# Optimization experiments

Measured on AMD Instinct MI355X. Metric: run time of the kernel, lower is better.

The kernel has to match this reference:

```python
import jax, jax.numpy as jnp
import numpy as np
from math import sqrt

B, S, F, H, FF, L = 16, 512, 512, 8, 2048, 3
HEAD_DIM = F // H
LN_EPS = 1e-5


def setup_inputs() -> dict:
    key = jax.random.key(0)
    ks = iter(jax.random.split(key, 80))

    def nrm(shape, scale=0.02):
        return jax.random.normal(next(ks), shape, jnp.float32) * scale

    inp = {
        "embedding": jax.random.normal(next(ks), (B, S, F), jnp.float32),
        "lengths": jax.random.randint(next(ks), (B,), 1, S + 1, dtype=jnp.int32),
    }
    for p in ("enc", "dec"):
        inp[p + "_wqkv"] = nrm((L, 3, F, F))
        inp[p + "_bqkv"] = nrm((L, 3, F))
        inp[p + "_wo"] = nrm((L, F, F))
        inp[p + "_bo"] = nrm((L, F))
        inp[p + "_ln1_g"] = jnp.ones((L, F), jnp.float32)
        inp[p + "_ln1_b"] = jnp.zeros((L, F), jnp.float32)
        inp[p + "_ff_w1"] = nrm((L, F, FF))
        inp[p + "_ff_b1"] = nrm((L, FF))
        inp[p + "_ff_w2"] = nrm((L, FF, F))
        inp[p + "_ff_b2"] = nrm((L, F))
        inp[p + "_ln2_g"] = jnp.ones((L, F), jnp.float32)
        inp[p + "_ln2_b"] = jnp.zeros((L, F), jnp.float32)
    inp["ptr_w_q"] = nrm((F,), 1.0)
    inp["ptr_w_k"] = nrm((F,), 1.0)
    return inp


def _ln(x, g, b):
    mu = x.mean(-1, keepdims=True)
    var = ((x - mu) ** 2).mean(-1, keepdims=True)
    return (x - mu) / jnp.sqrt(var + LN_EPS) * g + b


def _mha(q_in, kv_in, wqkv, bqkv, wo, bo, mask):
    # q_in [b,sq,f], kv_in [b,sk,f], mask broadcastable to [b,h,sq,sk] (True = masked)
    b, sq, f = q_in.shape
    q = q_in @ wqkv[0] + bqkv[0]
    k = kv_in @ wqkv[1] + bqkv[1]
    v = kv_in @ wqkv[2] + bqkv[2]

    def split(t):
        return t.reshape(t.shape[0], t.shape[1], H, HEAD_DIM).transpose(0, 2, 1, 3)

    q, k, v = split(q), split(k), split(v)  # [b,h,s,dh]
    scores = jnp.einsum("bhqd,bhkd->bhqk", q, k) / sqrt(HEAD_DIM)
    scores = jnp.where(mask, jnp.finfo(scores.dtype).min, scores)
    attn = jax.nn.softmax(scores, axis=-1)
    out = jnp.einsum("bhqk,bhkd->bhqd", attn, v)
    out = out.transpose(0, 2, 1, 3).reshape(b, sq, f)
    return out @ wo + bo


def _layer(x, mem, mask, wqkv, bqkv, wo, bo, ln1_g, ln1_b, w1, b1, w2, b2, ln2_g, ln2_b):
    x = _ln(x + _mha(x, mem, wqkv, bqkv, wo, bo, mask), ln1_g, ln1_b)
    ff = jax.nn.gelu(x @ w1 + b1, approximate=False) @ w2 + b2
    return _ln(x + ff, ln2_g, ln2_b)


def _forward(embedding, lengths,
             enc_wqkv, enc_bqkv, enc_wo, enc_bo, enc_ln1_g, enc_ln1_b,
             enc_ff_w1, enc_ff_b1, enc_ff_w2, enc_ff_b2, enc_ln2_g, enc_ln2_b,
             dec_wqkv, dec_bqkv, dec_wo, dec_bo, dec_ln1_g, dec_ln1_b,
             dec_ff_w1, dec_ff_b1, dec_ff_w2, dec_ff_b2, dec_ln2_g, dec_ln2_b,
             ptr_w_q, ptr_w_k):
    b, s, f = embedding.shape
    pos = jnp.arange(s)
    key_mask = pos[None, :] >= lengths[:, None]  # [b,s] True = padded

    # ---- encoder (self-attn with key padding mask) ----
    enc_mask = key_mask[:, None, None, :]  # [b,1,1,s]
    x = embedding
    for i in range(L):
        x = _layer(x, x, enc_mask,
                   enc_wqkv[i], enc_bqkv[i], enc_wo[i], enc_bo[i],
                   enc_ln1_g[i], enc_ln1_b[i],
                   enc_ff_w1[i], enc_ff_b1[i], enc_ff_w2[i], enc_ff_b2[i],
                   enc_ln2_g[i], enc_ln2_b[i])
    memory = x

    # ---- decoder: all timesteps batched (no recurrent state in original loop) ----
    # query t attends keys j < min(t, len); t=0 is overridden with zeros below
    # (key 0 left unmasked for t=0 only to keep softmax finite).
    t = jnp.arange(s)
    limit = jnp.minimum(jnp.maximum(t, 1)[None, :], lengths[:, None])  # [b,sq]
    dec_mask = (pos[None, None, :] >= limit[:, :, None])[:, None, :, :]  # [b,1,sq,sk]
    y = embedding
    for i in range(L):
        y = _layer(y, memory, dec_mask,
                   dec_wqkv[i], dec_bqkv[i], dec_wo[i], dec_bo[i],
                   dec_ln1_g[i], dec_ln1_b[i],
                   dec_ff_w1[i], dec_ff_b1[i], dec_ff_w2[i], dec_ff_b2[i],
                   dec_ln2_g[i], dec_ln2_b[i])

    # ---- pointer logits ----
    wq = y @ ptr_w_q        # [b, sq]
    wk = memory @ ptr_w_k   # [b, sk]
    ptr = jax.nn.sigmoid((wq[:, None, :] + wk[:, :, None]) / sqrt(f))  # [b, sk, sq]
    return jnp.where(t[None, None, :] == 0, 0.0, ptr)


def reference(embedding, lengths,
              enc_wqkv, enc_bqkv, enc_wo, enc_bo, enc_ln1_g, enc_ln1_b,
              enc_ff_w1, enc_ff_b1, enc_ff_w2, enc_ff_b2, enc_ln2_g, enc_ln2_b,
              dec_wqkv, dec_bqkv, dec_wo, dec_bo, dec_ln1_g, dec_ln1_b,
              dec_ff_w1, dec_ff_b1, dec_ff_w2, dec_ff_b2, dec_ln2_g, dec_ln2_b,
              ptr_w_q, ptr_w_k):
    return _forward(embedding, lengths,
                    enc_wqkv, enc_bqkv, enc_wo, enc_bo, enc_ln1_g, enc_ln1_b,
                    enc_ff_w1, enc_ff_b1, enc_ff_w2, enc_ff_b2, enc_ln2_g, enc_ln2_b,
                    dec_wqkv, dec_bqkv, dec_wo, dec_bo, dec_ln1_g, dec_ln1_b,
                    dec_ff_w1, dec_ff_b1, dec_ff_w2, dec_ff_b2, dec_ln2_g, dec_ln2_b,
                    ptr_w_q, ptr_w_k)
```

## Files before the change

### kernel.cpp

```cpp
#include <hip/hip_runtime.h>
#include <hip/hip_bf16.h>
#include <math.h>

#define TB 16
#define TS 512
#define TF 512
#define TH 8
#define TFF 2048
#define TL 3

typedef unsigned short u16;
typedef short bf16x8 __attribute__((ext_vector_type(8)));
typedef float f32x4 __attribute__((ext_vector_type(4)));

__device__ __forceinline__ u16 f2b(float f) {
    __hip_bfloat16 h = __float2bfloat16(f);
    return *reinterpret_cast<u16*>(&h);
}
__device__ __forceinline__ float b2f(u16 u) {
    unsigned int v = ((unsigned int)u) << 16;
    return __builtin_bit_cast(float, v);
}

__device__ __forceinline__ void gload_lds16(const void* g, void* l) {
    __builtin_amdgcn_global_load_lds(
        (const __attribute__((address_space(1))) unsigned int*)g,
        (__attribute__((address_space(3))) unsigned int*)l, 16, 0, 0);
}

__global__ __launch_bounds__(256) void k_transpose_w(
    const float* __restrict__ src, u16* __restrict__ dst, int K, int N)
{
    __shared__ float tile[32][33];
    const int z = blockIdx.z;
    src += (size_t)z * K * N;
    dst += (size_t)z * K * N;
    const int n0 = blockIdx.x * 32, k0 = blockIdx.y * 32;
    const int tx = threadIdx.x & 31, ty = threadIdx.x >> 5;
    #pragma unroll
    for (int i = 0; i < 32; i += 8)
        tile[ty + i][tx] = src[(size_t)(k0 + ty + i) * N + n0 + tx];
    __syncthreads();
    #pragma unroll
    for (int i = 0; i < 32; i += 8)
        dst[(size_t)(n0 + ty + i) * K + k0 + tx] = f2b(tile[tx][ty + i]);
}

__global__ __launch_bounds__(256) void k_cvt(
    const float* __restrict__ src, u16* __restrict__ d16, int n4)
{
    const int i = blockIdx.x * 256 + threadIdx.x;
    if (i >= n4) return;
    float4 v = ((const float4*)src)[i];
    ushort4 p;
    p.x = f2b(v.x); p.y = f2b(v.y); p.z = f2b(v.z); p.w = f2b(v.w);
    ((ushort4*)d16)[i] = p;
}

template<int EPI, int BN>
__global__ __launch_bounds__(512, 1) void k_g8(
    const u16* __restrict__ A, const u16* __restrict__ A2, int asplit,
    const u16* __restrict__ BT,
    const float* __restrict__ bias, const u16* __restrict__ residb,
    u16* __restrict__ outb,
    u16* __restrict__ out_k, u16* __restrict__ out_v,
    int N, int K, int ldo, int coloff)
{
    constexpr int NFB = BN / 64;
    __shared__ __align__(16) u16 SH[2 * 128 * 64 + 2 * BN * 64];
    u16* Asm = SH;
    u16* Bsm = SH + 2 * 128 * 64;

    const int gx = gridDim.x;
    int bid = blockIdx.y * gx + blockIdx.x;
    const int cpx = (gx * gridDim.y) >> 3;
    bid = (bid & 7) * cpx + (bid >> 3);
    const int bn = bid % gx, bm = bid / gx;

    const int t = threadIdx.x;
    const int w = t >> 6, l = t & 63;
    const int wm = w >> 2, wn = w & 3;
    const int lhi = l >> 4, llo = l & 15;

    f32x4 acc[4][NFB];
    #pragma unroll
    for (int m = 0; m < 4; ++m)
        #pragma unroll
        for (int n = 0; n < NFB; ++n)
            acc[m][n] = f32x4{0.f, 0.f, 0.f, 0.f};

    const u16* Asrc = (bn * BN < asplit) ? A : A2;
    const int lr = l >> 3;
    const int lcz = ((l & 7) ^ lr) * 8;
    const u16* Ag = Asrc + (size_t)(bm * 128 + w * 8 + lr) * K + lcz;
    const u16* Bg = BT + (size_t)(bn * BN + w * 8 + lr) * K + lcz;

    auto stage = [&](int buf, int tt) {
        const int kofs = tt << 6;
        gload_lds16(Ag + kofs,          Asm + buf * 8192 + (w * 8) * 64);
        gload_lds16(Ag + 64 * K + kofs, Asm + buf * 8192 + (64 + w * 8) * 64);
        #pragma unroll
        for (int i = 0; i < BN / 64; ++i)
            gload_lds16(Bg + (size_t)i * 64 * K + kofs,
                        Bsm + buf * (BN * 64) + (i * 64 + w * 8) * 64);
    };

    const int NT = K >> 6;
    stage(0, 0);
    stage(1, 1);
    for (int tt = 0; tt < NT; ++tt) {
        const int cur = tt & 1;
        if (tt + 1 < NT) {
            if constexpr (BN == 256) asm volatile("s_waitcnt vmcnt(6)" ::: "memory");
            else                     asm volatile("s_waitcnt vmcnt(4)" ::: "memory");
        } else {
            asm volatile("s_waitcnt vmcnt(0)" ::: "memory");
        }
        __builtin_amdgcn_s_barrier();
        __builtin_amdgcn_sched_barrier(0);

        bf16x8 af[4][2], bfr[NFB][2];
        #pragma unroll
        for (int m = 0; m < 4; ++m) {
            const int row = wm * 64 + m * 16 + llo;
            const int x = row & 7;
            af[m][0] = *(const bf16x8*)(Asm + cur * 8192 + row * 64 + ((lhi) ^ x) * 8);
            af[m][1] = *(const bf16x8*)(Asm + cur * 8192 + row * 64 + ((4 + lhi) ^ x) * 8);
        }
        #pragma unroll
        for (int n = 0; n < NFB; ++n) {
            const int row = wn * (BN / 4) + n * 16 + llo;
            const int x = row & 7;
            bfr[n][0] = *(const bf16x8*)(Bsm + cur * (BN * 64) + row * 64 + ((lhi) ^ x) * 8);
            bfr[n][1] = *(const bf16x8*)(Bsm + cur * (BN * 64) + row * 64 + ((4 + lhi) ^ x) * 8);
        }
        asm volatile("s_waitcnt lgkmcnt(0)" ::: "memory");
        __builtin_amdgcn_sched_barrier(0);
        __builtin_amdgcn_s_setprio(1);
        #pragma unroll
        for (int m = 0; m < 2; ++m)
            #pragma unroll
            for (int n = 0; n < NFB; ++n) {
                acc[m][n] = __builtin_amdgcn_mfma_f32_16x16x32_bf16(af[m][0], bfr[n][0], acc[m][n], 0, 0, 0);
                acc[m][n] = __builtin_amdgcn_mfma_f32_16x16x32_bf16(af[m][1], bfr[n][1], acc[m][n], 0, 0, 0);
            }
        __builtin_amdgcn_s_setprio(0);
        __builtin_amdgcn_sched_barrier(0);
        __builtin_amdgcn_s_barrier();
        if (tt + 2 < NT) stage(cur, tt + 2);
        __builtin_amdgcn_s_setprio(1);
        #pragma unroll
        for (int m = 2; m < 4; ++m)
            #pragma unroll
            for (int n = 0; n < NFB; ++n) {
                acc[m][n] = __builtin_amdgcn_mfma_f32_16x16x32_bf16(af[m][0], bfr[n][0], acc[m][n], 0, 0, 0);
                acc[m][n] = __builtin_amdgcn_mfma_f32_16x16x32_bf16(af[m][1], bfr[n][1], acc[m][n], 0, 0, 0);
            }
        __builtin_amdgcn_s_setprio(0);
    }

    const int colb = bn * BN + wn * (BN / 4);
    const int rowb = bm * 128 + wm * 64 + lhi * 4;
    const int c0w = coloff + colb;

    if constexpr (EPI == 3 && BN == 256) {
        if (c0w >= 1024) {
            u16* tb = SH + w * 4096;
            #pragma unroll
            for (int n = 0; n < 4; ++n) {
                const int dl = n * 16 + llo;
                const float bv = bias[colb + n * 16 + llo];
                #pragma unroll
                for (int m = 0; m < 4; ++m) {
                    ushort4 pk;
                    #pragma unroll
                    for (int r = 0; r < 4; ++r)
                        ((u16*)&pk)[r] = f2b(acc[m][n][r] + bv);
                    const int slc = m * 2 + (lhi >> 1);
                    const int addr = dl * 64 + ((slc ^ (dl & 7)) << 3) + ((lhi & 1) << 2);
                    *(ushort4*)(tb + addr) = pk;
                }
            }
            asm volatile("s_waitcnt lgkmcnt(0)" ::: "memory");
            __builtin_amdgcn_sched_barrier(0);
            const int sbase = bm * 128 + wm * 64;
            const int bidx = sbase >> 9;
            const int srem = sbase & 511;
            const int hh = (c0w >> 6) & 7;
            u16* vo = out_v + ((size_t)bidx * 8 + hh) * 32768 + srem;
            const int cchunk = l & 7;
            #pragma unroll
            for (int rr = 0; rr < 8; ++rr) {
                const int dl2 = (l >> 3) + rr * 8;
                const int ch = cchunk ^ (dl2 & 7);
                bf16x8 vv = *(const bf16x8*)(tb + dl2 * 64 + ch * 8);
                *(bf16x8*)(vo + (size_t)dl2 * 512 + cchunk * 8) = vv;
            }
            return;
        }
    }

    #pragma unroll
    for (int n = 0; n < NFB; ++n) {
        const int col = colb + n * 16 + llo;
        const float bv = bias[col];
        #pragma unroll
        for (int m = 0; m < 4; ++m) {
            const int row = rowb + m * 16;
            if (EPI == 3) {
                float vv[4];
                #pragma unroll
                for (int r = 0; r < 4; ++r) vv[r] = acc[m][n][r] + bv;
                const int c = coloff + col;
                if ((c >> 9) == 0) {
                    #pragma unroll
                    for (int r = 0; r < 4; ++r)
                        outb[(size_t)(row + r) * 512 + c] = f2b(vv[r]);
                } else {
                    const int hh = (c >> 6) & 7, d = c & 63;
                    #pragma unroll
                    for (int r = 0; r < 4; ++r) {
                        const int rr = row + r;
                        out_k[((size_t)(rr >> 9) * 8 + hh) * 32768 + (rr & 511) * 64 + d] = f2b(vv[r]);
                    }
                }
            } else {
                #pragma unroll
                for (int r = 0; r < 4; ++r) {
                    float v = acc[m][n][r] + bv;
                    const size_t off = (size_t)(row + r) * ldo + coloff + col;
                    if (EPI == 0) {
                        outb[off] = f2b(v);
                    } else if (EPI == 1) {
                        v = 0.5f * v * (1.f + erff(v * 0.70710678118654752f));
                        outb[off] = f2b(v);
                    } else {
                        v += b2f(residb[off]);
                        outb[off] = f2b(v);
                    }
                }
            }
        }
    }
}

template<int DEC>
__global__ __launch_bounds__(256) void k_attn(
    const u16* __restrict__ qb, const u16* __restrict__ kc,
    const u16* __restrict__ vtp, const int* __restrict__ lengths,
    u16* __restrict__ out)
{
    __shared__ __align__(16) u16 Ks[2][64 * 64];
    __shared__ __align__(16) u16 Vs[2][64 * 64];
    __shared__ __align__(16) u16 plds[4][16][64];
    __shared__ float alds[4][16];
    __shared__ float llds[4][16];
    const int qt = blockIdx.x;
    const int bh = blockIdx.y;
    const int b = bh >> 3;
    const int h = bh & 7;
    const int t = threadIdx.x, w = t >> 6, l = t & 63;
    const int lhi = l >> 4, llo = l & 15;
    const int len = lengths[b];
    const int qrow0 = qt * 64 + w * 16;
    const int q = qrow0 + llo;

    const u16* qp = qb + (size_t)(b * TS + q) * 512 + h * 64 + lhi * 8;
    bf16x8 qf0 = *(const bf16x8*)(qp);
    bf16x8 qf1 = *(const bf16x8*)(qp + 32);

    const u16* kb = kc  + (size_t)bh * 32768;
    const u16* vb = vtp + (size_t)bh * 32768;

    const int qlim = DEC ? min(max(q, 1), len) : len;
    const int limb = DEC ? min(qt * 64 + 63, len) : len;
    const int ktend = (limb + 63) >> 6;

    f32x4 o[4];
    #pragma unroll
    for (int g = 0; g < 4; ++g) o[g] = f32x4{0.f, 0.f, 0.f, 0.f};
    float mrun = -1e30f, lrun = 0.f;

    const float SC = 0.18033688011112042f;

    const int sr = w * 8 + (l >> 3);
    const int sc = (((l & 7) ^ (sr & 7)) << 3);
    auto stage = [&](int buf, int ktt) {
        gload_lds16(kb + ((ktt * 64 + sr) << 6) + sc,        &Ks[buf][(w * 8) * 64]);
        gload_lds16(kb + ((ktt * 64 + 32 + sr) << 6) + sc,   &Ks[buf][(32 + w * 8) * 64]);
        gload_lds16(vb + (size_t)sr * 512 + ktt * 64 + sc,   &Vs[buf][(w * 8) * 64]);
        gload_lds16(vb + (size_t)(32 + sr) * 512 + ktt * 64 + sc, &Vs[buf][(32 + w * 8) * 64]);
    };

    stage(0, 0);
    for (int kt = 0; kt < ktend; ++kt) {
        const int cur = kt & 1;
        if (kt + 1 < ktend) {
            stage(cur ^ 1, kt + 1);
            asm volatile("s_waitcnt vmcnt(4)" ::: "memory");
        } else {
            asm volatile("s_waitcnt vmcnt(0)" ::: "memory");
        }
        __builtin_amdgcn_s_barrier();
        __builtin_amdgcn_sched_barrier(0);

        bf16x8 kf[4][2], vf[4][2];
        #pragma unroll
        for (int g = 0; g < 4; ++g) {
            const int row = g * 16 + llo;
            const int x = row & 7;
            kf[g][0] = *(const bf16x8*)&Ks[cur][row * 64 + ((lhi) ^ x) * 8];
            kf[g][1] = *(const bf16x8*)&Ks[cur][row * 64 + ((4 + lhi) ^ x) * 8];
            vf[g][0] = *(const bf16x8*)&Vs[cur][row * 64 + ((lhi) ^ x) * 8];
            vf[g][1] = *(const bf16x8*)&Vs[cur][row * 64 + ((4 + lhi) ^ x) * 8];
        }
        f32x4 s[4];
        #pragma unroll
        for (int g = 0; g < 4; ++g) {
            s[g] = f32x4{0.f, 0.f, 0.f, 0.f};
            s[g] = __builtin_amdgcn_mfma_f32_16x16x32_bf16(kf[g][0], qf0, s[g], 0, 0, 0);
            s[g] = __builtin_amdgcn_mfma_f32_16x16x32_bf16(kf[g][1], qf1, s[g], 0, 0, 0);
        }
        #pragma unroll
        for (int g = 0; g < 4; ++g) {
            const int key = kt * 64 + g * 16 + lhi * 4;
            #pragma unroll
            for (int r = 0; r < 4; ++r)
                s[g][r] = (key + r < qlim) ? s[g][r] * SC : -1e30f;
        }
        float tm = fmaxf(fmaxf(fmaxf(s[0][0], s[0][1]), fmaxf(s[0][2], s[0][3])),
                         fmaxf(fmaxf(s[1][0], s[1][1]), fmaxf(s[1][2], s[1][3])));
        tm = fmaxf(tm, fmaxf(fmaxf(fmaxf(s[2][0], s[2][1]), fmaxf(s[2][2], s[2][3])),
                             fmaxf(fmaxf(s[3][0], s[3][1]), fmaxf(s[3][2], s[3][3]))));
        tm = fmaxf(tm, __shfl_xor(tm, 16));
        tm = fmaxf(tm, __shfl_xor(tm, 32));
        const float mnew = fmaxf(mrun, tm);
        const float alpha = exp2f(mrun - mnew);
        mrun = mnew;
        float rs = 0.f;
        ushort4 pk[4];
        #pragma unroll
        for (int g = 0; g < 4; ++g) {
            #pragma unroll
            for (int r = 0; r < 4; ++r) {
                const float p = exp2f(s[g][r] - mnew);
                rs += p;
                ((u16*)&pk[g])[r] = f2b(p);
            }
        }
        rs += __shfl_xor(rs, 16);
        rs += __shfl_xor(rs, 32);
        lrun = lrun * alpha + rs;
        if (lhi == 0) alds[w][llo] = alpha;
        #pragma unroll
        for (int g = 0; g < 4; ++g) {
            const int chw = (g * 2 + (lhi >> 1)) ^ (llo & 7);
            *(ushort4*)((char*)&plds[w][0][0] + llo * 128 + chw * 16 + (lhi & 1) * 8) = pk[g];
        }
        const float4 av = *(const float4*)&alds[w][lhi * 4];
        #pragma unroll
        for (int g = 0; g < 4; ++g) {
            o[g][0] *= av.x; o[g][1] *= av.y; o[g][2] *= av.z; o[g][3] *= av.w;
        }
        #pragma unroll
        for (int ks = 0; ks < 2; ++ks) {
            const int chr = (ks * 4 + lhi) ^ (llo & 7);
            bf16x8 pa = *(const bf16x8*)((const char*)&plds[w][0][0] + llo * 128 + chr * 16);
            #pragma unroll
            for (int g = 0; g < 4; ++g)
                o[g] = __builtin_amdgcn_mfma_f32_16x16x32_bf16(pa, vf[g][ks], o[g], 0, 0, 0);
        }
        __builtin_amdgcn_sched_barrier(0);
        __builtin_amdgcn_s_barrier();
    }

    if (lhi == 0) llds[w][llo] = 1.f / lrun;
    __builtin_amdgcn_s_waitcnt(0);
    const float4 linv = *(const float4*)&llds[w][lhi * 4];
    #pragma unroll
    for (int g = 0; g < 4; ++g) {
        const int d = h * 64 + g * 16 + llo;
        #pragma unroll
        for (int r = 0; r < 4; ++r) {
            const int qq = qrow0 + lhi * 4 + r;
            out[(size_t)(b * TS + qq) * 512 + d] = f2b(o[g][r] * ((const float*)&linv)[r]);
        }
    }
}

__global__ __launch_bounds__(256) void k_ln(
    const u16* __restrict__ in, const float* __restrict__ gam,
    const float* __restrict__ bet, u16* __restrict__ o16,
    const float* __restrict__ dotv, float* __restrict__ dotout)
{
    const int row = blockIdx.x * 4 + (threadIdx.x >> 6);
    const int l = threadIdx.x & 63;
    bf16x8 vin = *(const bf16x8*)(in + (size_t)row * 512 + l * 8);
    float x[8];
    #pragma unroll
    for (int i = 0; i < 8; ++i) x[i] = b2f((u16)vin[i]);
    float s = x[0] + x[1] + x[2] + x[3] + x[4] + x[5] + x[6] + x[7];
    #pragma unroll
    for (int off = 32; off; off >>= 1) s += __shfl_xor(s, off);
    const float mu = s * (1.f / 512.f);
    float v = 0.f;
    #pragma unroll
    for (int i = 0; i < 8; ++i) { const float d = x[i] - mu; v += d * d; }
    #pragma unroll
    for (int off = 32; off; off >>= 1) v += __shfl_xor(v, off);
    const float rstd = rsqrtf(v * (1.f / 512.f) + 1e-5f);
    float gg[8], bb[8];
    *(float4*)&gg[0] = *(const float4*)(gam + l * 8);
    *(float4*)&gg[4] = *(const float4*)(gam + l * 8 + 4);
    *(float4*)&bb[0] = *(const float4*)(bet + l * 8);
    *(float4*)&bb[4] = *(const float4*)(bet + l * 8 + 4);
    float y[8];
    #pragma unroll
    for (int i = 0; i < 8; ++i) y[i] = (x[i] - mu) * rstd * gg[i] + bb[i];
    ushort4 pk0, pk1;
    pk0.x = f2b(y[0]); pk0.y = f2b(y[1]); pk0.z = f2b(y[2]); pk0.w = f2b(y[3]);
    pk1.x = f2b(y[4]); pk1.y = f2b(y[5]); pk1.z = f2b(y[6]); pk1.w = f2b(y[7]);
    ushort4* o16p = (ushort4*)(o16 + (size_t)row * 512 + l * 8);
    o16p[0] = pk0; o16p[1] = pk1;
    if (dotv) {
        float wa[8];
        *(float4*)&wa[0] = *(const float4*)(dotv + l * 8);
        *(float4*)&wa[4] = *(const float4*)(dotv + l * 8 + 4);
        float ds = 0.f;
        #pragma unroll
        for (int i = 0; i < 8; ++i) ds += y[i] * wa[i];
        #pragma unroll
        for (int off = 32; off; off >>= 1) ds += __shfl_xor(ds, off);
        if (l == 0) dotout[row] = ds;
    }
}

__global__ __launch_bounds__(256) void k_ptr_out(
    const float* __restrict__ wq, const float* __restrict__ wk, float* __restrict__ out)
{
    const int bi = blockIdx.x;
    const int b = bi >> 9;
    const float wki = wk[bi];
    #pragma unroll
    for (int j = threadIdx.x; j < 512; j += 256) {
        float r = 0.f;
        if (j != 0) {
            const float z = (wq[b * 512 + j] + wki) * 0.044194173824159216f;
            r = 1.f / (1.f + __expf(-z));
        }
        out[(size_t)bi * 512 + j] = r;
    }
}

extern "C" void kernel_launch(void* const* d_in, const int* in_sizes, int n_in,
                              void* d_out, int out_size, void* d_ws, size_t ws_size,
                              hipStream_t stream)
{
    const float* emb = (const float*)d_in[0];
    const int* lengths = (const int*)d_in[1];
    struct Pw {
        const float *wqkv, *bqkv, *wo, *bo, *ln1g, *ln1b, *w1, *b1, *w2, *b2, *ln2g, *ln2b;
    } pp[2];
    for (int p = 0; p < 2; ++p) {
        const int base = 2 + p * 12;
        pp[p].wqkv = (const float*)d_in[base + 0];
        pp[p].bqkv = (const float*)d_in[base + 1];
        pp[p].wo   = (const float*)d_in[base + 2];
        pp[p].bo   = (const float*)d_in[base + 3];
        pp[p].ln1g = (const float*)d_in[base + 4];
        pp[p].ln1b = (const float*)d_in[base + 5];
        pp[p].w1   = (const float*)d_in[base + 6];
        pp[p].b1   = (const float*)d_in[base + 7];
        pp[p].w2   = (const float*)d_in[base + 8];
        pp[p].b2   = (const float*)d_in[base + 9];
        pp[p].ln2g = (const float*)d_in[base + 10];
        pp[p].ln2b = (const float*)d_in[base + 11];
    }
    const float* pwq = (const float*)d_in[26];
    const float* pwk = (const float*)d_in[27];

    char* ws = (char*)d_ws;
    auto alloc = [&](size_t bytes) {
        char* p = ws;
        ws += (bytes + 255) & ~(size_t)255;
        return p;
    };
    u16* wqkvT[2], *woT[2], *w1T[2], *w2T[2];
    for (int p = 0; p < 2; ++p) {
        wqkvT[p] = (u16*)alloc((size_t)TL * 1536 * 512 * 2);
        woT[p]   = (u16*)alloc((size_t)TL * 512 * 512 * 2);
        w1T[p]   = (u16*)alloc((size_t)TL * 2048 * 512 * 2);
        w2T[p]   = (u16*)alloc((size_t)TL * 512 * 2048 * 2);
    }
    const size_t MR = (size_t)TB * TS;
    u16*   x16   = (u16*)alloc(MR * 512 * 2);
    u16*   mem16 = (u16*)alloc(MR * 512 * 2);
    u16*   pre16 = (u16*)alloc(MR * 512 * 2);
    u16*   qbuf  = (u16*)alloc(MR * 512 * 2);
    u16*   kcb   = (u16*)alloc((size_t)TB * TH * 512 * 64 * 2);
    u16*   vtb   = (u16*)alloc((size_t)TB * TH * 64 * 512 * 2);
    u16*   att16 = (u16*)alloc(MR * 512 * 2);
    u16*   h16   = (u16*)alloc(MR * 2048 * 2);
    float* wqb   = (float*)alloc(MR * 4);
    float* wkb   = (float*)alloc(MR * 4);

    for (int p = 0; p < 2; ++p) {
        k_transpose_w<<<dim3(16, 16, 9), 256, 0, stream>>>(pp[p].wqkv, wqkvT[p], 512, 512);
        k_transpose_w<<<dim3(16, 16, 3), 256, 0, stream>>>(pp[p].wo, woT[p], 512, 512);
        k_transpose_w<<<dim3(64, 16, 3), 256, 0, stream>>>(pp[p].w1, w1T[p], 512, 2048);
        k_transpose_w<<<dim3(16, 64, 3), 256, 0, stream>>>(pp[p].w2, w2T[p], 2048, 512);
    }

    const int n4 = (int)(MR * 512 / 4);
    k_cvt<<<4096, 256, 0, stream>>>(emb, x16, n4);

    for (int i = 0; i < TL; ++i) {
        k_g8<3, 256><<<dim3(6, 64), 512, 0, stream>>>(
            x16, x16, 1536, wqkvT[0] + (size_t)i * 1536 * 512, pp[0].bqkv + i * 1536,
            nullptr, qbuf, kcb, vtb, 1536, 512, 1536, 0);
        k_attn<0><<<dim3(8, 128), 256, 0, stream>>>(qbuf, kcb, vtb, lengths, att16);
        k_g8<2, 128><<<dim3(4, 64), 512, 0, stream>>>(
            att16, att16, 512, woT[0] + (size_t)i * 512 * 512, pp[0].bo + i * 512,
            x16, pre16, nullptr, nullptr, 512, 512, 512, 0);
        k_ln<<<2048, 256, 0, stream>>>(pre16, pp[0].ln1g + i * 512, pp[0].ln1b + i * 512,
                                       x16, nullptr, nullptr);
        k_g8<1, 256><<<dim3(8, 64), 512, 0, stream>>>(
            x16, x16, 2048, w1T[0] + (size_t)i * 2048 * 512, pp[0].b1 + i * 2048,
            nullptr, h16, nullptr, nullptr, 2048, 512, 2048, 0);
        k_g8<2, 128><<<dim3(4, 64), 512, 0, stream>>>(
            h16, h16, 512, w2T[0] + (size_t)i * 512 * 2048, pp[0].b2 + i * 512,
            x16, pre16, nullptr, nullptr, 512, 2048, 512, 0);
        if (i == TL - 1)
            k_ln<<<2048, 256, 0, stream>>>(pre16, pp[0].ln2g + i * 512, pp[0].ln2b + i * 512,
                                           mem16, pwk, wkb);
        else
            k_ln<<<2048, 256, 0, stream>>>(pre16, pp[0].ln2g + i * 512, pp[0].ln2b + i * 512,
                                           x16, nullptr, nullptr);
    }
    k_cvt<<<4096, 256, 0, stream>>>(emb, x16, n4);

    for (int i = 0; i < TL; ++i) {
        k_g8<3, 256><<<dim3(6, 64), 512, 0, stream>>>(
            x16, mem16, 512, wqkvT[1] + (size_t)i * 1536 * 512, pp[1].bqkv + i * 1536,
            nullptr, qbuf, kcb, vtb, 1536, 512, 1536, 0);
        k_attn<1><<<dim3(8, 128), 256, 0, stream>>>(qbuf, kcb, vtb, lengths, att16);
        k_g8<2, 128><<<dim3(4, 64), 512, 0, stream>>>(
            att16, att16, 512, woT[1] + (size_t)i * 512 * 512, pp[1].bo + i * 512,
            x16, pre16, nullptr, nullptr, 512, 512, 512, 0);
        k_ln<<<2048, 256, 0, stream>>>(pre16, pp[1].ln1g + i * 512, pp[1].ln1b + i * 512,
                                       x16, nullptr, nullptr);
        k_g8<1, 256><<<dim3(8, 64), 512, 0, stream>>>(
            x16, x16, 2048, w1T[1] + (size_t)i * 2048 * 512, pp[1].b1 + i * 2048,
            nullptr, h16, nullptr, nullptr, 2048, 512, 2048, 0);
        k_g8<2, 128><<<dim3(4, 64), 512, 0, stream>>>(
            h16, h16, 512, w2T[1] + (size_t)i * 512 * 2048, pp[1].b2 + i * 512,
            x16, pre16, nullptr, nullptr, 512, 2048, 512, 0);
        if (i == TL - 1)
            k_ln<<<2048, 256, 0, stream>>>(pre16, pp[1].ln2g + i * 512, pp[1].ln2b + i * 512,
                                           x16, pwq, wqb);
        else
            k_ln<<<2048, 256, 0, stream>>>(pre16, pp[1].ln2g + i * 512, pp[1].ln2b + i * 512,
                                           x16, nullptr, nullptr);
    }

    k_ptr_out<<<TB * TS, 256, 0, stream>>>(wqb, wkb, (float*)d_out);
}
```

Measured before the change: 873.5 us.

## Triple-buffer GEMM LDS pipeline with split-phase fragment loads, reuse converted embedding

The GEMM main loop moves from two LDS buffers to three, so the prefetch for tile tt+2 can be issued right after the barrier instead of halfway through the MFMA work. Fragment reads are split per k-half, and for BN=256 also per m-half, each followed by a barrier and its MFMA batch, to interleave LDS reads with matrix math. Separately, the embedding is converted to bf16 once into its own buffer and used by both encoder and decoder, which drops the second conversion kernel. This costs more LDS per block and adds barriers, plus an extra barrier before the epilogue reuses shared memory.

```diff
diff --git a/kernel.cpp b/kernel.cpp
--- a/kernel.cpp
+++ b/kernel.cpp
@@ -67,9 +67,9 @@
     int N, int K, int ldo, int coloff)
 {
     constexpr int NFB = BN / 64;
-    __shared__ __align__(16) u16 SH[2 * 128 * 64 + 2 * BN * 64];
+    __shared__ __align__(16) u16 SH[3 * 128 * 64 + 3 * BN * 64];
     u16* Asm = SH;
-    u16* Bsm = SH + 2 * 128 * 64;
+    u16* Bsm = SH + 3 * 128 * 64;
 
     const int gx = gridDim.x;
     int bid = blockIdx.y * gx + blockIdx.x;
@@ -108,8 +108,8 @@
     const int NT = K >> 6;
     stage(0, 0);
     stage(1, 1);
+    int cur = 0;
     for (int tt = 0; tt < NT; ++tt) {
-        const int cur = tt & 1;
         if (tt + 1 < NT) {
             if constexpr (BN == 256) asm volatile("s_waitcnt vmcnt(6)" ::: "memory");
             else                     asm volatile("s_waitcnt vmcnt(4)" ::: "memory");
@@ -118,45 +118,81 @@
         }
         __builtin_amdgcn_s_barrier();
         __builtin_amdgcn_sched_barrier(0);
-
+        if (tt + 2 < NT) {
+            int nb = cur + 2; if (nb >= 3) nb -= 3;
+            stage(nb, tt + 2);
+        }
+
+        const u16* Ab = Asm + cur * 8192;
+        const u16* Bb = Bsm + cur * (BN * 64);
         bf16x8 af[4][2], bfr[NFB][2];
-        #pragma unroll
-        for (int m = 0; m < 4; ++m) {
-            const int row = wm * 64 + m * 16 + llo;
-            const int x = row & 7;
-            af[m][0] = *(const bf16x8*)(Asm + cur * 8192 + row * 64 + ((lhi) ^ x) * 8);
-            af[m][1] = *(const bf16x8*)(Asm + cur * 8192 + row * 64 + ((4 + lhi) ^ x) * 8);
-        }
-        #pragma unroll
-        for (int n = 0; n < NFB; ++n) {
-            const int row = wn * (BN / 4) + n * 16 + llo;
-            const int x = row & 7;
-            bfr[n][0] = *(const bf16x8*)(Bsm + cur * (BN * 64) + row * 64 + ((lhi) ^ x) * 8);
-            bfr[n][1] = *(const bf16x8*)(Bsm + cur * (BN * 64) + row * 64 + ((4 + lhi) ^ x) * 8);
-        }
-        asm volatile("s_waitcnt lgkmcnt(0)" ::: "memory");
-        __builtin_amdgcn_sched_barrier(0);
-        __builtin_amdgcn_s_setprio(1);
-        #pragma unroll
-        for (int m = 0; m < 2; ++m)
+
+        if constexpr (BN == 256) {
             #pragma unroll
-            for (int n = 0; n < NFB; ++n) {
-                acc[m][n] = __builtin_amdgcn_mfma_f32_16x16x32_bf16(af[m][0], bfr[n][0], acc[m][n], 0, 0, 0);
-                acc[m][n] = __builtin_amdgcn_mfma_f32_16x16x32_bf16(af[m][1], bfr[n][1], acc[m][n], 0, 0, 0);
+            for (int kk = 0; kk < 2; ++kk) {
+                #pragma unroll
+                for (int mh = 0; mh < 2; ++mh) {
+                    #pragma unroll
+                    for (int mi = 0; mi < 2; ++mi) {
+                        const int m = mh * 2 + mi;
+                        const int row = wm * 64 + m * 16 + llo;
+                        const int x = row & 7;
+                        af[m][kk] = *(const bf16x8*)(Ab + row * 64 + ((kk * 4 + lhi) ^ x) * 8);
+                    }
+                    if (mh == 0) {
+                        #pragma unroll
+                        for (int n = 0; n < NFB; ++n) {
+                            const int row = wn * (BN / 4) + n * 16 + llo;
+                            const int x = row & 7;
+                            bfr[n][kk] = *(const bf16x8*)(Bb + row * 64 + ((kk * 4 + lhi) ^ x) * 8);
+                        }
+                    }
+                    __builtin_amdgcn_s_barrier();
+                    asm volatile("s_waitcnt lgkmcnt(0)" ::: "memory");
+                    __builtin_amdgcn_sched_barrier(0);
+                    __builtin_amdgcn_s_setprio(1);
+                    #pragma unroll
+                    for (int mi = 0; mi < 2; ++mi) {
+                        const int m = mh * 2 + mi;
+                        #pragma unroll
+                        for (int n = 0; n < NFB; ++n)
+                            acc[m][n] = __builtin_amdgcn_mfma_f32_16x16x32_bf16(
+                                af[m][kk], bfr[n][kk], acc[m][n], 0, 0, 0);
+                    }
+                    __builtin_amdgcn_s_setprio(0);
+                    __builtin_amdgcn_sched_barrier(0);
+                }
             }
-        __builtin_amdgcn_s_setprio(0);
-        __builtin_amdgcn_sched_barrier(0);
-        __builtin_amdgcn_s_barrier();
-        if (tt + 2 < NT) stage(cur, tt + 2);
-        __builtin_amdgcn_s_setprio(1);
-        #pragma unroll
-        for (int m = 2; m < 4; ++m)
+        } else {
             #pragma unroll
-            for (int n = 0; n < NFB; ++n) {
-                acc[m][n] = __builtin_amdgcn_mfma_f32_16x16x32_bf16(af[m][0], bfr[n][0], acc[m][n], 0, 0, 0);
-                acc[m][n] = __builtin_amdgcn_mfma_f32_16x16x32_bf16(af[m][1], bfr[n][1], acc[m][n], 0, 0, 0);
+            for (int kk = 0; kk < 2; ++kk) {
+                #pragma unroll
+                for (int m = 0; m < 4; ++m) {
+                    const int row = wm * 64 + m * 16 + llo;
+                    const int x = row & 7;
+                    af[m][kk] = *(const bf16x8*)(Ab + row * 64 + ((kk * 4 + lhi) ^ x) * 8);
+                }
+                #pragma unroll
+                for (int n = 0; n < NFB; ++n) {
+                    const int row = wn * (BN / 4) + n * 16 + llo;
+                    const int x = row & 7;
+                    bfr[n][kk] = *(const bf16x8*)(Bb + row * 64 + ((kk * 4 + lhi) ^ x) * 8);
+                }
+                __builtin_amdgcn_s_barrier();
+                asm volatile("s_waitcnt lgkmcnt(0)" ::: "memory");
+                __builtin_amdgcn_sched_barrier(0);
+                __builtin_amdgcn_s_setprio(1);
+                #pragma unroll
+                for (int m = 0; m < 4; ++m)
+                    #pragma unroll
+                    for (int n = 0; n < NFB; ++n)
+                        acc[m][n] = __builtin_amdgcn_mfma_f32_16x16x32_bf16(
+                            af[m][kk], bfr[n][kk], acc[m][n], 0, 0, 0);
+                __builtin_amdgcn_s_setprio(0);
+                __builtin_amdgcn_sched_barrier(0);
             }
-        __builtin_amdgcn_s_setprio(0);
+        }
+        ++cur; if (cur >= 3) cur = 0;
     }
 
     const int colb = bn * BN + wn * (BN / 4);
@@ -165,6 +201,7 @@
 
     if constexpr (EPI == 3 && BN == 256) {
         if (c0w >= 1024) {
+            __builtin_amdgcn_s_barrier();
             u16* tb = SH + w * 4096;
             #pragma unroll
             for (int n = 0; n < 4; ++n) {
@@ -493,6 +530,7 @@
         w2T[p]   = (u16*)alloc((size_t)TL * 512 * 2048 * 2);
     }
     const size_t MR = (size_t)TB * TS;
+    u16*   emb16 = (u16*)alloc(MR * 512 * 2);
     u16*   x16   = (u16*)alloc(MR * 512 * 2);
     u16*   mem16 = (u16*)alloc(MR * 512 * 2);
     u16*   pre16 = (u16*)alloc(MR * 512 * 2);
@@ -512,16 +550,17 @@
     }
 
     const int n4 = (int)(MR * 512 / 4);
-    k_cvt<<<4096, 256, 0, stream>>>(emb, x16, n4);
+    k_cvt<<<4096, 256, 0, stream>>>(emb, emb16, n4);
 
     for (int i = 0; i < TL; ++i) {
+        const u16* xin = (i == 0) ? emb16 : x16;
         k_g8<3, 256><<<dim3(6, 64), 512, 0, stream>>>(
-            x16, x16, 1536, wqkvT[0] + (size_t)i * 1536 * 512, pp[0].bqkv + i * 1536,
+            xin, xin, 1536, wqkvT[0] + (size_t)i * 1536 * 512, pp[0].bqkv + i * 1536,
             nullptr, qbuf, kcb, vtb, 1536, 512, 1536, 0);
         k_attn<0><<<dim3(8, 128), 256, 0, stream>>>(qbuf, kcb, vtb, lengths, att16);
         k_g8<2, 128><<<dim3(4, 64), 512, 0, stream>>>(
             att16, att16, 512, woT[0] + (size_t)i * 512 * 512, pp[0].bo + i * 512,
-            x16, pre16, nullptr, nullptr, 512, 512, 512, 0);
+            xin, pre16, nullptr, nullptr, 512, 512, 512, 0);
         k_ln<<<2048, 256, 0, stream>>>(pre16, pp[0].ln1g + i * 512, pp[0].ln1b + i * 512,
                                        x16, nullptr, nullptr);
         k_g8<1, 256><<<dim3(8, 64), 512, 0, stream>>>(
@@ -537,16 +576,16 @@
             k_ln<<<2048, 256, 0, stream>>>(pre16, pp[0].ln2g + i * 512, pp[0].ln2b + i * 512,
                                            x16, nullptr, nullptr);
     }
-    k_cvt<<<4096, 256, 0, stream>>>(emb, x16, n4);
 
     for (int i = 0; i < TL; ++i) {
+        const u16* yin = (i == 0) ? emb16 : x16;
         k_g8<3, 256><<<dim3(6, 64), 512, 0, stream>>>(
-            x16, mem16, 512, wqkvT[1] + (size_t)i * 1536 * 512, pp[1].bqkv + i * 1536,
+            yin, mem16, 512, wqkvT[1] + (size_t)i * 1536 * 512, pp[1].bqkv + i * 1536,
             nullptr, qbuf, kcb, vtb, 1536, 512, 1536, 0);
         k_attn<1><<<dim3(8, 128), 256, 0, stream>>>(qbuf, kcb, vtb, lengths, att16);
         k_g8<2, 128><<<dim3(4, 64), 512, 0, stream>>>(
             att16, att16, 512, woT[1] + (size_t)i * 512 * 512, pp[1].bo + i * 512,
-            x16, pre16, nullptr, nullptr, 512, 512, 512, 0);
+            yin, pre16, nullptr, nullptr, 512, 512, 512, 0);
         k_ln<<<2048, 256, 0, stream>>>(pre16, pp[1].ln1g + i * 512, pp[1].ln1b + i * 512,
                                        x16, nullptr, nullptr);
         k_g8<1, 256><<<dim3(8, 64), 512, 0, stream>>>(
```

Result: faster. 849.2 us (-2.8%).

## Use 256x256 GEMM tiles for QKV and FF1, reuse converted embedding

Applied to the files above, without the earlier changes.

Parameterizes the bf16 MFMA GEMM by a BM tile height and switches the QKV and FF1 projections to 256x256 tiles with a 4x2 wave layout, which halves the grid and raises operand reuse per block. The main loop now issues all MFMAs after the LDS reloads instead of splitting them around the barrier. Launch bounds now allow two blocks per CU. The embedding is converted to bf16 once into a separate buffer shared by the encoder and decoder, removing the second conversion. Larger tiles raise register and LDS use and leave fewer blocks to fill the CUs.

```diff
diff --git a/kernel.cpp b/kernel.cpp
--- a/kernel.cpp
+++ b/kernel.cpp
@@ -57,8 +57,8 @@
     ((ushort4*)d16)[i] = p;
 }
 
-template<int EPI, int BN>
-__global__ __launch_bounds__(512, 1) void k_g8(
+template<int EPI, int BM, int BN>
+__global__ __launch_bounds__(512, 2) void k_g8(
     const u16* __restrict__ A, const u16* __restrict__ A2, int asplit,
     const u16* __restrict__ BT,
     const float* __restrict__ bias, const u16* __restrict__ residb,
@@ -66,10 +66,14 @@
     u16* __restrict__ out_k, u16* __restrict__ out_v,
     int N, int K, int ldo, int coloff)
 {
-    constexpr int NFB = BN / 64;
-    __shared__ __align__(16) u16 SH[2 * 128 * 64 + 2 * BN * 64];
+    constexpr int WN  = (BM == 256) ? 2 : 4;
+    constexpr int CS  = BN / WN;
+    constexpr int NFB = CS / 16;
+    constexpr int NLA = BM / 64, NLB = BN / 64;
+    constexpr int NL  = NLA + NLB;
+    __shared__ __align__(16) u16 SH[2 * BM * 64 + 2 * BN * 64];
     u16* Asm = SH;
-    u16* Bsm = SH + 2 * 128 * 64;
+    u16* Bsm = SH + 2 * BM * 64;
 
     const int gx = gridDim.x;
     int bid = blockIdx.y * gx + blockIdx.x;
@@ -79,7 +83,7 @@
 
     const int t = threadIdx.x;
     const int w = t >> 6, l = t & 63;
-    const int wm = w >> 2, wn = w & 3;
+    const int wm = w / WN, wn = w % WN;
     const int lhi = l >> 4, llo = l & 15;
 
     f32x4 acc[4][NFB];
@@ -92,15 +96,17 @@
     const u16* Asrc = (bn * BN < asplit) ? A : A2;
     const int lr = l >> 3;
     const int lcz = ((l & 7) ^ lr) * 8;
-    const u16* Ag = Asrc + (size_t)(bm * 128 + w * 8 + lr) * K + lcz;
+    const u16* Ag = Asrc + (size_t)(bm * BM + w * 8 + lr) * K + lcz;
     const u16* Bg = BT + (size_t)(bn * BN + w * 8 + lr) * K + lcz;
 
     auto stage = [&](int buf, int tt) {
         const int kofs = tt << 6;
-        gload_lds16(Ag + kofs,          Asm + buf * 8192 + (w * 8) * 64);
-        gload_lds16(Ag + 64 * K + kofs, Asm + buf * 8192 + (64 + w * 8) * 64);
-        #pragma unroll
-        for (int i = 0; i < BN / 64; ++i)
+        #pragma unroll
+        for (int i = 0; i < NLA; ++i)
+            gload_lds16(Ag + (size_t)i * 64 * K + kofs,
+                        Asm + buf * (BM * 64) + (i * 64 + w * 8) * 64);
+        #pragma unroll
+        for (int i = 0; i < NLB; ++i)
             gload_lds16(Bg + (size_t)i * 64 * K + kofs,
                         Bsm + buf * (BN * 64) + (i * 64 + w * 8) * 64);
     };
@@ -111,90 +117,93 @@
     for (int tt = 0; tt < NT; ++tt) {
         const int cur = tt & 1;
         if (tt + 1 < NT) {
-            if constexpr (BN == 256) asm volatile("s_waitcnt vmcnt(6)" ::: "memory");
-            else                     asm volatile("s_waitcnt vmcnt(4)" ::: "memory");
+            if constexpr (NL == 8) asm volatile("s_waitcnt vmcnt(8)" ::: "memory");
+            else                   asm volatile("s_waitcnt vmcnt(4)" ::: "memory");
         } else {
             asm volatile("s_waitcnt vmcnt(0)" ::: "memory");
         }
         __builtin_amdgcn_s_barrier();
         __builtin_amdgcn_sched_barrier(0);
 
+        const u16* Ab = Asm + cur * (BM * 64);
+        const u16* Bb = Bsm + cur * (BN * 64);
         bf16x8 af[4][2], bfr[NFB][2];
         #pragma unroll
         for (int m = 0; m < 4; ++m) {
             const int row = wm * 64 + m * 16 + llo;
             const int x = row & 7;
-            af[m][0] = *(const bf16x8*)(Asm + cur * 8192 + row * 64 + ((lhi) ^ x) * 8);
-            af[m][1] = *(const bf16x8*)(Asm + cur * 8192 + row * 64 + ((4 + lhi) ^ x) * 8);
+            af[m][0] = *(const bf16x8*)(Ab + row * 64 + ((lhi) ^ x) * 8);
+            af[m][1] = *(const bf16x8*)(Ab + row * 64 + ((4 + lhi) ^ x) * 8);
         }
         #pragma unroll
         for (int n = 0; n < NFB; ++n) {
-            const int row = wn * (BN / 4) + n * 16 + llo;
+            const int row = wn * CS + n * 16 + llo;
             const int x = row & 7;
-            bfr[n][0] = *(const bf16x8*)(Bsm + cur * (BN * 64) + row * 64 + ((lhi) ^ x) * 8);
-            bfr[n][1] = *(const bf16x8*)(Bsm + cur * (BN * 64) + row * 64 + ((4 + lhi) ^ x) * 8);
+            bfr[n][0] = *(const bf16x8*)(Bb + row * 64 + ((lhi) ^ x) * 8);
+            bfr[n][1] = *(const bf16x8*)(Bb + row * 64 + ((4 + lhi) ^ x) * 8);
         }
         asm volatile("s_waitcnt lgkmcnt(0)" ::: "memory");
-        __builtin_amdgcn_sched_barrier(0);
-        __builtin_amdgcn_s_setprio(1);
-        #pragma unroll
-        for (int m = 0; m < 2; ++m)
-            #pragma unroll
-            for (int n = 0; n < NFB; ++n) {
-                acc[m][n] = __builtin_amdgcn_mfma_f32_16x16x32_bf16(af[m][0], bfr[n][0], acc[m][n], 0, 0, 0);
-                acc[m][n] = __builtin_amdgcn_mfma_f32_16x16x32_bf16(af[m][1], bfr[n][1], acc[m][n], 0, 0, 0);
-            }
-        __builtin_amdgcn_s_setprio(0);
         __builtin_amdgcn_sched_barrier(0);
         __builtin_amdgcn_s_barrier();
         if (tt + 2 < NT) stage(cur, tt + 2);
         __builtin_amdgcn_s_setprio(1);
         #pragma unroll
-        for (int m = 2; m < 4; ++m)
+        for (int kk = 0; kk < 2; ++kk)
             #pragma unroll
-            for (int n = 0; n < NFB; ++n) {
-                acc[m][n] = __builtin_amdgcn_mfma_f32_16x16x32_bf16(af[m][0], bfr[n][0], acc[m][n], 0, 0, 0);
-                acc[m][n] = __builtin_amdgcn_mfma_f32_16x16x32_bf16(af[m][1], bfr[n][1], acc[m][n], 0, 0, 0);
-            }
+            for (int m = 0; m < 4; ++m)
+                #pragma unroll
+                for (int n = 0; n < NFB; ++n)
+                    acc[m][n] = __builtin_amdgcn_mfma_f32_16x16x32_bf16(
+                        af[m][kk], bfr[n][kk], acc[m][n], 0, 0, 0);
         __builtin_amdgcn_s_setprio(0);
-    }
-
-    const int colb = bn * BN + wn * (BN / 4);
-    const int rowb = bm * 128 + wm * 64 + lhi * 4;
+        __builtin_amdgcn_sched_barrier(0);
+    }
+
+    const int colb = bn * BN + wn * CS;
+    const int rowb = bm * BM + wm * 64 + lhi * 4;
     const int c0w = coloff + colb;
 
-    if constexpr (EPI == 3 && BN == 256) {
+    if constexpr (EPI == 3 && BM == 256) {
         if (c0w >= 1024) {
-            u16* tb = SH + w * 4096;
+            __builtin_amdgcn_s_barrier();
+            u16* tb = SH + w * 8192;
             #pragma unroll
-            for (int n = 0; n < 4; ++n) {
-                const int dl = n * 16 + llo;
-                const float bv = bias[colb + n * 16 + llo];
+            for (int nh = 0; nh < 2; ++nh) {
                 #pragma unroll
-                for (int m = 0; m < 4; ++m) {
-                    ushort4 pk;
+                for (int ni = 0; ni < 4; ++ni) {
+                    const int n = nh * 4 + ni;
+                    const int dl = ni * 16 + llo;
+                    const float bv = bias[colb + n * 16 + llo];
                     #pragma unroll
-                    for (int r = 0; r < 4; ++r)
-                        ((u16*)&pk)[r] = f2b(acc[m][n][r] + bv);
-                    const int slc = m * 2 + (lhi >> 1);
-                    const int addr = dl * 64 + ((slc ^ (dl & 7)) << 3) + ((lhi & 1) << 2);
-                    *(ushort4*)(tb + addr) = pk;
+                    for (int m = 0; m < 4; ++m) {
+                        ushort4 pk;
+                        #pragma unroll
+                        for (int r = 0; r < 4; ++r)
+                            ((u16*)&pk)[r] = f2b(acc[m][n][r] + bv);
+                        const int slc = m * 2 + (lhi >> 1);
+                        const int addr = nh * 4096 + dl * 64
+                                       + ((slc ^ (dl & 7)) << 3) + ((lhi & 1) << 2);
+                        *(ushort4*)(tb + addr) = pk;
+                    }
                 }
             }
             asm volatile("s_waitcnt lgkmcnt(0)" ::: "memory");
             __builtin_amdgcn_sched_barrier(0);
-            const int sbase = bm * 128 + wm * 64;
+            const int sbase = bm * BM + wm * 64;
             const int bidx = sbase >> 9;
             const int srem = sbase & 511;
-            const int hh = (c0w >> 6) & 7;
-            u16* vo = out_v + ((size_t)bidx * 8 + hh) * 32768 + srem;
             const int cchunk = l & 7;
             #pragma unroll
-            for (int rr = 0; rr < 8; ++rr) {
-                const int dl2 = (l >> 3) + rr * 8;
-                const int ch = cchunk ^ (dl2 & 7);
-                bf16x8 vv = *(const bf16x8*)(tb + dl2 * 64 + ch * 8);
-                *(bf16x8*)(vo + (size_t)dl2 * 512 + cchunk * 8) = vv;
+            for (int nh = 0; nh < 2; ++nh) {
+                const int hh = (((c0w >> 6) + nh) & 7);
+                u16* vo = out_v + ((size_t)bidx * 8 + hh) * 32768 + srem;
+                #pragma unroll
+                for (int rr = 0; rr < 8; ++rr) {
+                    const int dl2 = (l >> 3) + rr * 8;
+                    const int ch = cchunk ^ (dl2 & 7);
+                    bf16x8 vv = *(const bf16x8*)(tb + nh * 4096 + dl2 * 64 + ch * 8);
+                    *(bf16x8*)(vo + (size_t)dl2 * 512 + cchunk * 8) = vv;
+                }
             }
             return;
         }
@@ -493,6 +502,7 @@
         w2T[p]   = (u16*)alloc((size_t)TL * 512 * 2048 * 2);
     }
     const size_t MR = (size_t)TB * TS;
+    u16*   emb16 = (u16*)alloc(MR * 512 * 2);
     u16*   x16   = (u16*)alloc(MR * 512 * 2);
     u16*   mem16 = (u16*)alloc(MR * 512 * 2);
     u16*   pre16 = (u16*)alloc(MR * 512 * 2);
@@ -512,22 +522,23 @@
     }
 
     const int n4 = (int)(MR * 512 / 4);
-    k_cvt<<<4096, 256, 0, stream>>>(emb, x16, n4);
+    k_cvt<<<4096, 256, 0, stream>>>(emb, emb16, n4);
 
     for (int i = 0; i < TL; ++i) {
-        k_g8<3, 256><<<dim3(6, 64), 512, 0, stream>>>(
-            x16, x16, 1536, wqkvT[0] + (size_t)i * 1536 * 512, pp[0].bqkv + i * 1536,
+        const u16* xin = (i == 0) ? emb16 : x16;
+        k_g8<3, 256, 256><<<dim3(6, 32), 512, 0, stream>>>(
+            xin, xin, 1536, wqkvT[0] + (size_t)i * 1536 * 512, pp[0].bqkv + i * 1536,
             nullptr, qbuf, kcb, vtb, 1536, 512, 1536, 0);
         k_attn<0><<<dim3(8, 128), 256, 0, stream>>>(qbuf, kcb, vtb, lengths, att16);
-        k_g8<2, 128><<<dim3(4, 64), 512, 0, stream>>>(
+        k_g8<2, 128, 128><<<dim3(4, 64), 512, 0, stream>>>(
             att16, att16, 512, woT[0] + (size_t)i * 512 * 512, pp[0].bo + i * 512,
-            x16, pre16, nullptr, nullptr, 512, 512, 512, 0);
+            xin, pre16, nullptr, nullptr, 512, 512, 512, 0);
         k_ln<<<2048, 256, 0, stream>>>(pre16, pp[0].ln1g + i * 512, pp[0].ln1b + i * 512,
                                        x16, nullptr, nullptr);
-        k_g8<1, 256><<<dim3(8, 64), 512, 0, stream>>>(
+        k_g8<1, 256, 256><<<dim3(8, 32), 512, 0, stream>>>(
             x16, x16, 2048, w1T[0] + (size_t)i * 2048 * 512, pp[0].b1 + i * 2048,
             nullptr, h16, nullptr, nullptr, 2048, 512, 2048, 0);
-        k_g8<2, 128><<<dim3(4, 64), 512, 0, stream>>>(
+        k_g8<2, 128, 128><<<dim3(4, 64), 512, 0, stream>>>(
             h16, h16, 512, w2T[0] + (size_t)i * 512 * 2048, pp[0].b2 + i * 512,
             x16, pre16, nullptr, nullptr, 512, 2048, 512, 0);
         if (i == TL - 1)
@@ -537,22 +548,22 @@
             k_ln<<<2048, 256, 0, stream>>>(pre16, pp[0].ln2g + i * 512, pp[0].ln2b + i * 512,
                                            x16, nullptr, nullptr);
     }
-    k_cvt<<<4096, 256, 0, stream>>>(emb, x16, n4);
 
     for (int i = 0; i < TL; ++i) {
-        k_g8<3, 256><<<dim3(6, 64), 512, 0, stream>>>(
-            x16, mem16, 512, wqkvT[1] + (size_t)i * 1536 * 512, pp[1].bqkv + i * 1536,
+        const u16* yin = (i == 0) ? emb16 : x16;
+        k_g8<3, 256, 256><<<dim3(6, 32), 512, 0, stream>>>(
+            yin, mem16, 512, wqkvT[1] + (size_t)i * 1536 * 512, pp[1].bqkv + i * 1536,
             nullptr, qbuf, kcb, vtb, 1536, 512, 1536, 0);
         k_attn<1><<<dim3(8, 128), 256, 0, stream>>>(qbuf, kcb, vtb, lengths, att16);
-        k_g8<2, 128><<<dim3(4, 64), 512, 0, stream>>>(
+        k_g8<2, 128, 128><<<dim3(4, 64), 512, 0, stream>>>(
             att16, att16, 512, woT[1] + (size_t)i * 512 * 512, pp[1].bo + i * 512,
-            x16, pre16, nullptr, nullptr, 512, 512, 512, 0);
+            yin, pre16, nullptr, nullptr, 512, 512, 512, 0);
         k_ln<<<2048, 256, 0, stream>>>(pre16, pp[1].ln1g + i * 512, pp[1].ln1b + i * 512,
                                        x16, nullptr, nullptr);
-        k_g8<1, 256><<<dim3(8, 64), 512, 0, stream>>>(
+        k_g8<1, 256, 256><<<dim3(8, 32), 512, 0, stream>>>(
             x16, x16, 2048, w1T[1] + (size_t)i * 2048 * 512, pp[1].b1 + i * 2048,
             nullptr, h16, nullptr, nullptr, 2048, 512, 2048, 0);
-        k_g8<2, 128><<<dim3(4, 64), 512, 0, stream>>>(
+        k_g8<2, 128, 128><<<dim3(4, 64), 512, 0, stream>>>(
             h16, h16, 512, w2T[1] + (size_t)i * 512 * 2048, pp[1].b2 + i * 512,
             x16, pre16, nullptr, nullptr, 512, 2048, 512, 0);
         if (i == TL - 1)
```

Result: faster. 836.5 us (-4.2%).
